# Kernel optimization log

Measured on AMD Instinct MI355X. Metric: run time of the kernel, lower is better.

Reference implementation:

```python
import jax, jax.numpy as jnp
import numpy as np

TEMPERATURE = 0.07


def setup_inputs() -> dict:
    key = jax.random.key(0)
    k1, k2 = jax.random.split(key)
    B, V, C, H, W = 4, 2, 128, 32, 32
    features = jax.random.normal(k1, (B, V, C, H, W), dtype=jnp.float32)
    # L2-normalize per-pixel feature vectors (channel dim), as contrastive
    # embeddings are in practice; the original exp() is unstabilized.
    features = features / jnp.linalg.norm(features, axis=2, keepdims=True)
    labels = jax.random.randint(k2, (B, V, H, W), 0, 4, dtype=jnp.int32)
    return {"features": features, "labels": labels}


def reference(features, labels):
    B, V, C, H, W = features.shape
    # torch.cat(torch.unbind(features, dim=1), dim=0): views stacked along batch
    cf = jnp.transpose(features, (1, 0, 2, 3, 4)).reshape(B * V, C, H, W)
    # kernels = cf.permute(0,2,3,1).reshape(-1, C, 1, 1); conv2d with 1x1 kernels
    # == pairwise dot products of per-pixel feature vectors.
    X = jnp.transpose(cf, (0, 2, 3, 1)).reshape(-1, C)  # [N, C], N = B*V*H*W
    N = X.shape[0]
    logits = (X @ X.T) / TEMPERATURE  # [N, N]

    lab = jnp.transpose(labels, (1, 0, 2, 3)).reshape(-1)  # [N]
    mask = (lab[:, None] == lab[None, :]).astype(logits.dtype)  # [N, N]
    logits_mask = 1.0 - jnp.eye(N, dtype=logits.dtype)  # zero the diagonal
    mask = mask * logits_mask

    exp_logits = jnp.exp(logits) * logits_mask
    log_prob = logits - jnp.log(jnp.sum(exp_logits, axis=1, keepdims=True))
    mean_log_prob_pos = jnp.sum(mask * log_prob, axis=1) / jnp.sum(mask, axis=1)
    loss = -mean_log_prob_pos  # [N]

    non_bg = (lab != 0).astype(logits.dtype)
    return jnp.sum(loss * non_bg) / jnp.sum(non_bg)
```

## Files before the change

### kernel.cpp

```cpp
#include <hip/hip_runtime.h>
#include <hip/hip_bf16.h>
#include <stdint.h>

typedef short bf16x8 __attribute__((ext_vector_type(8)));
typedef float f32x16 __attribute__((ext_vector_type(16)));

#define NROWS 8192
#define CDIM  128
#define TEMP  0.07f
#define C1F   20.6099291555566248f

#define OFF_S    0
#define OFF_G    32768
#define OFF_HIST (32768 + 2048)
#define OFF_SUM  (32768 + 2048 + 16)
#define OFF_TKT  (32768 + 2048 + 16 + 4)
#define ZBYTES   (32768 + 2048 + 16 + 4 + 4)
#define ZWORDS   (ZBYTES / 4)
#define OFF_GPART (ZBYTES + 8)
#define OFF_CPART (OFF_GPART + 256 * 512 * 4)

__device__ __forceinline__ float bf2f(unsigned short u) {
  union { unsigned int i; float f; } x; x.i = ((unsigned int)u) << 16; return x.f;
}
__device__ __forceinline__ unsigned short f2bf(float f) {
  union { float f; unsigned int i; } x; x.f = f;
  unsigned int r = x.i + 0x7fffu + ((x.i >> 16) & 1u);
  return (unsigned short)(r >> 16);
}
__device__ __forceinline__ float fexp2(float x) {
#if __has_builtin(__builtin_amdgcn_exp2f)
  return __builtin_amdgcn_exp2f(x);
#else
  return exp2f(x);
#endif
}

__global__ __launch_bounds__(256) void k_pack(const float* __restrict__ F,
                                              const int* __restrict__ labels,
                                              unsigned short* __restrict__ Xb,
                                              float* __restrict__ zbase,
                                              float* __restrict__ Gpart,
                                              int* __restrict__ Cpart) {
  const int tid = threadIdx.x;
  {
    int idx = blockIdx.x * 256 + tid;
    if (idx < ZWORDS) zbase[idx] = 0.0f;
  }
  __shared__ float lds[128 * 33];
  __shared__ int   slab[32];
  __shared__ float gred[4][128];
  const int g   = blockIdx.x >> 5;
  const int hw0 = (blockIdx.x & 31) << 5;
  if (tid < 32) slab[tid] = labels[g * 1024 + hw0 + tid];
#pragma unroll
  for (int p = 0; p < 16; ++p) {
    int c  = p * 8 + (tid >> 5);
    int hw = hw0 + (tid & 31);
    lds[c * 33 + (tid & 31)] = F[(g * 128 + c) * 1024 + hw];
  }
  __syncthreads();
#pragma unroll
  for (int p = 0; p < 16; ++p) {
    int hwl = p * 2 + (tid >> 7);
    int c   = tid & 127;
    int row = g * 1024 + hw0 + hwl;
    Xb[row * 128 + c] = f2bf(lds[c * 33 + hwl]);
  }
  const int c  = tid & 127;
  const int rh = tid >> 7;
  float a0 = 0.f, a1 = 0.f, a2 = 0.f, a3 = 0.f;
#pragma unroll
  for (int k = 0; k < 16; ++k) {
    int   hwl = rh * 16 + k;
    float v   = lds[c * 33 + hwl];
    int   lab = slab[hwl];
    a0 += (lab == 0) ? v : 0.f;
    a1 += (lab == 1) ? v : 0.f;
    a2 += (lab == 2) ? v : 0.f;
    a3 += (lab == 3) ? v : 0.f;
  }
  if (rh == 1) { gred[0][c] = a0; gred[1][c] = a1; gred[2][c] = a2; gred[3][c] = a3; }
  if (tid >= 32 && tid < 36) {
    int j = tid - 32, cnt = 0;
#pragma unroll
    for (int k2 = 0; k2 < 32; ++k2) cnt += (slab[k2] == j);
    Cpart[blockIdx.x * 4 + j] = cnt;
  }
  __syncthreads();
  if (rh == 0) {
    float* gp = Gpart + blockIdx.x * 512;
    gp[0 * 128 + c] = a0 + gred[0][c];
    gp[1 * 128 + c] = a1 + gred[1][c];
    gp[2 * 128 + c] = a2 + gred[2][c];
    gp[3 * 128 + c] = a3 + gred[3][c];
  }
}

__global__ __launch_bounds__(256, 2) void k_main(const unsigned short* __restrict__ Xb,
                                                 float* __restrict__ S,
                                                 float* __restrict__ G,
                                                 int* __restrict__ hist,
                                                 const float* __restrict__ Gpart,
                                                 const int* __restrict__ Cpart) {
  __shared__ int4 ldsB[2][2][16 * 33];
  const int bid  = blockIdx.x;
  const int tid  = threadIdx.x;
  const int lane = tid & 63;

  if (bid >= 512) {
    const int rb = bid - 512;
    const int l  = tid & 63;
    const int w  = tid >> 6;
    const float* gp = Gpart + (w * 64) * 512 + rb * 64 + l;
    float s = 0.f;
#pragma unroll 8
    for (int k = 0; k < 64; ++k) s += gp[k * 512];
    __shared__ float red[4][64];
    red[w][l] = s;
    __syncthreads();
    if (w == 0) G[rb * 64 + l] = red[0][l] + red[1][l] + red[2][l] + red[3][l];
    if (rb == 0) {
      int4 c4 = ((const int4*)Cpart)[tid];
      for (int mm = 1; mm < 64; mm <<= 1) {
        c4.x += __shfl_xor(c4.x, mm, 64);
        c4.y += __shfl_xor(c4.y, mm, 64);
        c4.z += __shfl_xor(c4.z, mm, 64);
        c4.w += __shfl_xor(c4.w, mm, 64);
      }
      __shared__ int hred[4][4];
      if (l == 0) { hred[w][0] = c4.x; hred[w][1] = c4.y; hred[w][2] = c4.z; hred[w][3] = c4.w; }
      __syncthreads();
      if (tid < 4) hist[tid] = hred[0][tid] + hred[1][tid] + hred[2][tid] + hred[3][tid];
    }
    return;
  }

  const int wave     = tid >> 6;
  const int rowBlock = bid >> 4;
  const int split    = bid & 15;
  const int r0       = rowBlock * 256 + wave * 64;
  const int col0     = split * 512;
  const int m        = lane & 31;
  const int half     = lane >> 5;

  bf16x8 afrag0[8], afrag1[8];
#pragma unroll
  for (int s = 0; s < 8; ++s) {
    afrag0[s] = *(const bf16x8*)(Xb + (r0 + m) * CDIM + (half + 2 * s) * 8);
    afrag1[s] = *(const bf16x8*)(Xb + (r0 + 32 + m) * CDIM + (half + 2 * s) * 8);
  }

  float accS0[16], accS1[16];
#pragma unroll
  for (int r = 0; r < 16; ++r) { accS0[r] = 0.f; accS1[r] = 0.f; }

  const int n_l = tid >> 3;
  const int bq  = tid & 7;
  const unsigned short* src = Xb + (col0 + n_l) * CDIM + bq * 16;
  int4 v0 = *(const int4*)src;
  int4 v1 = *(const int4*)(src + 8);
  int4 v2 = *(const int4*)(src + 32 * CDIM);
  int4 v3 = *(const int4*)(src + 32 * CDIM + 8);
  ldsB[0][0][(2 * bq) * 33 + n_l]     = v0;
  ldsB[0][0][(2 * bq + 1) * 33 + n_l] = v1;
  ldsB[0][1][(2 * bq) * 33 + n_l]     = v2;
  ldsB[0][1][(2 * bq + 1) * 33 + n_l] = v3;
  src += 64 * CDIM;
  v0 = *(const int4*)src;
  v1 = *(const int4*)(src + 8);
  v2 = *(const int4*)(src + 32 * CDIM);
  v3 = *(const int4*)(src + 32 * CDIM + 8);

  for (int t = 0; t < 8; ++t) {
    __syncthreads();
    if (t < 7) {
      const int nb = (t + 1) & 1;
      ldsB[nb][0][(2 * bq) * 33 + n_l]     = v0;
      ldsB[nb][0][(2 * bq + 1) * 33 + n_l] = v1;
      ldsB[nb][1][(2 * bq) * 33 + n_l]     = v2;
      ldsB[nb][1][(2 * bq + 1) * 33 + n_l] = v3;
    }
    if (t < 6) {
      src += 64 * CDIM;
      v0 = *(const int4*)src;
      v1 = *(const int4*)(src + 8);
      v2 = *(const int4*)(src + 32 * CDIM);
      v3 = *(const int4*)(src + 32 * CDIM + 8);
    }
    const int cur = t & 1;
#pragma unroll
    for (int u = 0; u < 2; ++u) {
      f32x16 acc0, acc1;
#pragma unroll
      for (int r = 0; r < 16; ++r) { acc0[r] = 0.f; acc1[r] = 0.f; }
#pragma unroll
      for (int s = 0; s < 8; ++s) {
        bf16x8 bfrag = *(const bf16x8*)&ldsB[cur][u][(half + 2 * s) * 33 + m];
        acc0 = __builtin_amdgcn_mfma_f32_32x32x16_bf16(afrag0[s], bfrag, acc0, 0, 0, 0);
        acc1 = __builtin_amdgcn_mfma_f32_32x32x16_bf16(afrag1[s], bfrag, acc1, 0, 0, 0);
      }
      const int colbase = col0 + t * 64 + u * 32;
      if (r0 == colbase) {
        const int colg = colbase + m;
#pragma unroll
        for (int r = 0; r < 16; ++r) {
          int   row = r0 + (r & 3) + 8 * (r >> 2) + 4 * half;
          float arg = (row == colg) ? -1e30f : acc0[r] * C1F;
          accS0[r] += fexp2(arg);
        }
      } else {
#pragma unroll
        for (int r = 0; r < 16; ++r) accS0[r] += fexp2(acc0[r] * C1F);
      }
      if (r0 + 32 == colbase) {
        const int colg = colbase + m;
#pragma unroll
        for (int r = 0; r < 16; ++r) {
          int   row = r0 + 32 + (r & 3) + 8 * (r >> 2) + 4 * half;
          float arg = (row == colg) ? -1e30f : acc1[r] * C1F;
          accS1[r] += fexp2(arg);
        }
      } else {
#pragma unroll
        for (int r = 0; r < 16; ++r) accS1[r] += fexp2(acc1[r] * C1F);
      }
    }
  }

#pragma unroll
  for (int r = 0; r < 16; ++r) {
    float v = accS0[r];
    v += __shfl_xor(v, 1, 64);
    v += __shfl_xor(v, 2, 64);
    v += __shfl_xor(v, 4, 64);
    v += __shfl_xor(v, 8, 64);
    v += __shfl_xor(v, 16, 64);
    accS0[r] = v;
    float v2 = accS1[r];
    v2 += __shfl_xor(v2, 1, 64);
    v2 += __shfl_xor(v2, 2, 64);
    v2 += __shfl_xor(v2, 4, 64);
    v2 += __shfl_xor(v2, 8, 64);
    v2 += __shfl_xor(v2, 16, 64);
    accS1[r] = v2;
  }
  if (m == 0) {
#pragma unroll
    for (int r = 0; r < 16; ++r) {
      int rowoff = (r & 3) + 8 * (r >> 2) + 4 * half;
      atomicAdd(&S[r0 + rowoff], accS0[r]);
      atomicAdd(&S[r0 + 32 + rowoff], accS1[r]);
    }
  }
}

__global__ __launch_bounds__(256) void k_loss(const unsigned short* __restrict__ Xb,
                                              const int* __restrict__ labels,
                                              const float* __restrict__ S,
                                              const float* __restrict__ G,
                                              const int* __restrict__ hist,
                                              float* __restrict__ sumLoss,
                                              int* __restrict__ ticket,
                                              float* __restrict__ out) {
  const int i   = blockIdx.x * 256 + threadIdx.x;
  const int lab = labels[i];
  const float* g = G + lab * 128;
  const unsigned short* x = Xb + i * CDIM;
  float dot = 0.f, nrm = 0.f;
#pragma unroll
  for (int cc = 0; cc < 16; ++cc) {
    int4 q = *(const int4*)(x + cc * 8);
    const unsigned int* qs = (const unsigned int*)&q;
#pragma unroll
    for (int j = 0; j < 4; ++j) {
      unsigned int u = qs[j];
      float lo = __uint_as_float(u << 16);
      float hi = __uint_as_float(u & 0xffff0000u);
      int   ci = cc * 8 + j * 2;
      dot += lo * g[ci] + hi * g[ci + 1];
      nrm += lo * lo + hi * hi;
    }
  }
  float Si   = S[i];
  float cnt  = (float)(hist[lab] - 1);
  float loss = logf(Si) - (dot - nrm) / (TEMP * cnt);
  float contrib = (lab != 0) ? loss : 0.f;
  for (int mm = 1; mm < 64; mm <<= 1) contrib += __shfl_xor(contrib, mm, 64);
  __shared__ float ws4[4];
  if ((threadIdx.x & 63) == 0) ws4[threadIdx.x >> 6] = contrib;
  __syncthreads();
  if (threadIdx.x == 0) {
    atomicAdd(sumLoss, ws4[0] + ws4[1] + ws4[2] + ws4[3]);
    __threadfence();
    int t = atomicAdd(ticket, 1);
    if (t == 31) {
      float total = atomicAdd(sumLoss, 0.0f);
      out[0] = total / (float)(NROWS - hist[0]);
    }
  }
}

extern "C" void kernel_launch(void* const* d_in, const int* in_sizes, int n_in,
                              void* d_out, int out_size, void* d_ws, size_t ws_size,
                              hipStream_t stream) {
  const float* F      = (const float*)d_in[0];
  const int*   labels = (const int*)d_in[1];
  char* ws = (char*)d_ws;

  unsigned short* Xb      = (unsigned short*)ws;
  const size_t    offS    = (size_t)NROWS * CDIM * 2;
  float*          S       = (float*)(ws + offS + OFF_S);
  float*          G       = (float*)(ws + offS + OFF_G);
  int*            hist    = (int*)(ws + offS + OFF_HIST);
  float*          sumLoss = (float*)(ws + offS + OFF_SUM);
  int*            ticket  = (int*)(ws + offS + OFF_TKT);
  float*          Gpart   = (float*)(ws + offS + OFF_GPART);
  int*            Cpart   = (int*)(ws + offS + OFF_CPART);

  hipLaunchKernelGGL(k_pack, dim3(256), dim3(256), 0, stream, F, labels, Xb, S, Gpart, Cpart);
  hipLaunchKernelGGL(k_main, dim3(520), dim3(256), 0, stream, Xb, S, G, hist, Gpart, Cpart);
  hipLaunchKernelGGL(k_loss, dim3(32), dim3(256), 0, stream, Xb, labels, S, G, hist,
                     sumLoss, ticket, (float*)d_out);
}
```

Baseline: 93.28 us.

## Exploit Gram matrix symmetry to compute only upper-triangular tiles

Reorganizes the row-sum-of-exp kernel to compute only the upper triangle of the symmetric X·Xᵀ matrix. Off-diagonal tile blocks are enumerated by triangular indexing and each tile's exp values feed both the row sums and the column sums, the latter through per-column atomics. Diagonal blocks are handled by paired waves that skip sub-diagonal sub-tiles. This roughly halves the MFMA and exp work, at the cost of more atomic traffic, a changed grid shape and per-wave load imbalance on the diagonal blocks.

```diff
diff --git a/kernel.cpp b/kernel.cpp
--- a/kernel.cpp
+++ b/kernel.cpp
@@ -136,28 +136,66 @@
     return;
   }
 
-  const int wave     = tid >> 6;
-  const int rowBlock = bid >> 4;
-  const int split    = bid & 15;
-  const int r0       = rowBlock * 256 + wave * 64;
-  const int col0     = split * 512;
-  const int m        = lane & 31;
-  const int half     = lane >> 5;
+  const int wave = tid >> 6;
+  const int m    = lane & 31;
+  const int half = lane >> 5;
+
+  int  rowA, rowB, colBase, NT;
+  bool isPair;
+  if (bid < 496) {
+    isPair = false;
+    const int k = bid;
+    int a = (int)((63.0f - sqrtf(3969.0f - 8.0f * (float)k)) * 0.5f);
+    while ((63 * (a + 1) - (a + 1) * (a + 1)) / 2 <= k) ++a;
+    while ((63 * a - a * a) / 2 > k) --a;
+    const int b = a + 1 + (k - (63 * a - a * a) / 2);
+    rowA    = a * 256 + wave * 32;
+    rowB    = a * 256 + (7 - wave) * 32;
+    colBase = b * 256;
+    NT      = 4;
+  } else {
+    isPair = true;
+    const int d = bid - 496;
+    rowA    = d * 512 + wave * 32;
+    rowB    = d * 512 + (7 - wave) * 32;
+    colBase = d * 512;
+    NT      = 8;
+  }
 
   bf16x8 afrag0[8], afrag1[8];
 #pragma unroll
   for (int s = 0; s < 8; ++s) {
-    afrag0[s] = *(const bf16x8*)(Xb + (r0 + m) * CDIM + (half + 2 * s) * 8);
-    afrag1[s] = *(const bf16x8*)(Xb + (r0 + 32 + m) * CDIM + (half + 2 * s) * 8);
+    afrag0[s] = *(const bf16x8*)(Xb + (rowA + m) * CDIM + (half + 2 * s) * 8);
+    afrag1[s] = *(const bf16x8*)(Xb + (rowB + m) * CDIM + (half + 2 * s) * 8);
   }
 
   float accS0[16], accS1[16];
 #pragma unroll
   for (int r = 0; r < 16; ++r) { accS0[r] = 0.f; accS1[r] = 0.f; }
+
+  auto flushRows = [&](int rA, int rB) {
+#pragma unroll
+    for (int r = 0; r < 16; ++r) {
+      float v = accS0[r];
+      v += __shfl_xor(v, 1, 64);  v += __shfl_xor(v, 2, 64);
+      v += __shfl_xor(v, 4, 64);  v += __shfl_xor(v, 8, 64);
+      v += __shfl_xor(v, 16, 64);
+      float v2 = accS1[r];
+      v2 += __shfl_xor(v2, 1, 64); v2 += __shfl_xor(v2, 2, 64);
+      v2 += __shfl_xor(v2, 4, 64); v2 += __shfl_xor(v2, 8, 64);
+      v2 += __shfl_xor(v2, 16, 64);
+      if (m == 0) {
+        int rowoff = (r & 3) + 8 * (r >> 2) + 4 * half;
+        atomicAdd(&S[rA + rowoff], v);
+        atomicAdd(&S[rB + rowoff], v2);
+      }
+      accS0[r] = 0.f; accS1[r] = 0.f;
+    }
+  };
 
   const int n_l = tid >> 3;
   const int bq  = tid & 7;
-  const unsigned short* src = Xb + (col0 + n_l) * CDIM + bq * 16;
+  const unsigned short* src = Xb + (colBase + n_l) * CDIM + bq * 16;
   int4 v0 = *(const int4*)src;
   int4 v1 = *(const int4*)(src + 8);
   int4 v2 = *(const int4*)(src + 32 * CDIM);
@@ -172,16 +210,25 @@
   v2 = *(const int4*)(src + 32 * CDIM);
   v3 = *(const int4*)(src + 32 * CDIM + 8);
 
-  for (int t = 0; t < 8; ++t) {
+  for (int t = 0; t < NT; ++t) {
     __syncthreads();
-    if (t < 7) {
+    if (isPair && t == 4) {
+      flushRows(rowA, rowB);
+      rowA += 256; rowB += 256;
+#pragma unroll
+      for (int s = 0; s < 8; ++s) {
+        afrag0[s] = *(const bf16x8*)(Xb + (rowA + m) * CDIM + (half + 2 * s) * 8);
+        afrag1[s] = *(const bf16x8*)(Xb + (rowB + m) * CDIM + (half + 2 * s) * 8);
+      }
+    }
+    if (t < NT - 1) {
       const int nb = (t + 1) & 1;
       ldsB[nb][0][(2 * bq) * 33 + n_l]     = v0;
       ldsB[nb][0][(2 * bq + 1) * 33 + n_l] = v1;
       ldsB[nb][1][(2 * bq) * 33 + n_l]     = v2;
       ldsB[nb][1][(2 * bq + 1) * 33 + n_l] = v3;
     }
-    if (t < 6) {
+    if (t < NT - 2) {
       src += 64 * CDIM;
       v0 = *(const int4*)src;
       v1 = *(const int4*)(src + 8);
@@ -191,68 +238,73 @@
     const int cur = t & 1;
 #pragma unroll
     for (int u = 0; u < 2; ++u) {
-      f32x16 acc0, acc1;
-#pragma unroll
-      for (int r = 0; r < 16; ++r) { acc0[r] = 0.f; acc1[r] = 0.f; }
-#pragma unroll
-      for (int s = 0; s < 8; ++s) {
-        bf16x8 bfrag = *(const bf16x8*)&ldsB[cur][u][(half + 2 * s) * 33 + m];
-        acc0 = __builtin_amdgcn_mfma_f32_32x32x16_bf16(afrag0[s], bfrag, acc0, 0, 0, 0);
-        acc1 = __builtin_amdgcn_mfma_f32_32x32x16_bf16(afrag1[s], bfrag, acc1, 0, 0, 0);
-      }
-      const int colbase = col0 + t * 64 + u * 32;
-      if (r0 == colbase) {
-        const int colg = colbase + m;
-#pragma unroll
-        for (int r = 0; r < 16; ++r) {
-          int   row = r0 + (r & 3) + 8 * (r >> 2) + 4 * half;
-          float arg = (row == colg) ? -1e30f : acc0[r] * C1F;
-          accS0[r] += fexp2(arg);
+      const int cb = (2 * t + u) & 7;
+      bool doA, doB, maskA, maskB;
+      if (isPair) {
+        doA = (cb >= wave);         maskA = (cb == wave);
+        doB = (cb >= 7 - wave);     maskB = (cb == 7 - wave);
+      } else {
+        doA = true; doB = true; maskA = false; maskB = false;
+      }
+      float csum = 0.f;
+      if (doA) {
+        f32x16 acc;
+#pragma unroll
+        for (int r = 0; r < 16; ++r) acc[r] = 0.f;
+#pragma unroll
+        for (int s = 0; s < 8; ++s) {
+          bf16x8 bfrag = *(const bf16x8*)&ldsB[cur][u][(half + 2 * s) * 33 + m];
+          acc = __builtin_amdgcn_mfma_f32_32x32x16_bf16(afrag0[s], bfrag, acc, 0, 0, 0);
         }
-      } else {
-#pragma unroll
-        for (int r = 0; r < 16; ++r) accS0[r] += fexp2(acc0[r] * C1F);
-      }
-      if (r0 + 32 == colbase) {
-        const int colg = colbase + m;
-#pragma unroll
-        for (int r = 0; r < 16; ++r) {
-          int   row = r0 + 32 + (r & 3) + 8 * (r >> 2) + 4 * half;
-          float arg = (row == colg) ? -1e30f : acc1[r] * C1F;
-          accS1[r] += fexp2(arg);
+        if (maskA) {
+#pragma unroll
+          for (int r = 0; r < 16; ++r) {
+            int rowoff = (r & 3) + 8 * (r >> 2) + 4 * half;
+            float e = (rowoff == m) ? 0.f : fexp2(acc[r] * C1F);
+            accS0[r] += e;
+          }
+        } else {
+#pragma unroll
+          for (int r = 0; r < 16; ++r) {
+            float e = fexp2(acc[r] * C1F);
+            accS0[r] += e;
+            csum += e;
+          }
         }
-      } else {
-#pragma unroll
-        for (int r = 0; r < 16; ++r) accS1[r] += fexp2(acc1[r] * C1F);
-      }
-    }
-  }
-
-#pragma unroll
-  for (int r = 0; r < 16; ++r) {
-    float v = accS0[r];
-    v += __shfl_xor(v, 1, 64);
-    v += __shfl_xor(v, 2, 64);
-    v += __shfl_xor(v, 4, 64);
-    v += __shfl_xor(v, 8, 64);
-    v += __shfl_xor(v, 16, 64);
-    accS0[r] = v;
-    float v2 = accS1[r];
-    v2 += __shfl_xor(v2, 1, 64);
-    v2 += __shfl_xor(v2, 2, 64);
-    v2 += __shfl_xor(v2, 4, 64);
-    v2 += __shfl_xor(v2, 8, 64);
-    v2 += __shfl_xor(v2, 16, 64);
-    accS1[r] = v2;
-  }
-  if (m == 0) {
-#pragma unroll
-    for (int r = 0; r < 16; ++r) {
-      int rowoff = (r & 3) + 8 * (r >> 2) + 4 * half;
-      atomicAdd(&S[r0 + rowoff], accS0[r]);
-      atomicAdd(&S[r0 + 32 + rowoff], accS1[r]);
-    }
-  }
+      }
+      if (doB) {
+        f32x16 acc;
+#pragma unroll
+        for (int r = 0; r < 16; ++r) acc[r] = 0.f;
+#pragma unroll
+        for (int s = 0; s < 8; ++s) {
+          bf16x8 bfrag = *(const bf16x8*)&ldsB[cur][u][(half + 2 * s) * 33 + m];
+          acc = __builtin_amdgcn_mfma_f32_32x32x16_bf16(afrag1[s], bfrag, acc, 0, 0, 0);
+        }
+        if (maskB) {
+#pragma unroll
+          for (int r = 0; r < 16; ++r) {
+            int rowoff = (r & 3) + 8 * (r >> 2) + 4 * half;
+            float e = (rowoff == m) ? 0.f : fexp2(acc[r] * C1F);
+            accS1[r] += e;
+          }
+        } else {
+#pragma unroll
+          for (int r = 0; r < 16; ++r) {
+            float e = fexp2(acc[r] * C1F);
+            accS1[r] += e;
+            csum += e;
+          }
+        }
+      }
+      if ((doA && !maskA) || (doB && !maskB)) {
+        float v = csum + __shfl_xor(csum, 32, 64);
+        if (half == 0) atomicAdd(&S[colBase + (2 * t + u) * 32 + m], v);
+      }
+    }
+  }
+
+  flushRows(rowA, rowB);
 }
 
 __global__ __launch_bounds__(256) void k_loss(const unsigned short* __restrict__ Xb,
```

Result: slower. 96.95 us (+3.9%).
